# Kernel optimization log

Measured on AMD Instinct MI355X. Metric: run time of the kernel, lower is better.

## Reference

```python
import jax, jax.numpy as jnp
import numpy as np

IH, IW = 48, 48           # img_size
C = 256                   # inp == oup
NH, HD = 8, 32            # num_heads, head_dims; inner_dim = 256
HID = 4 * C               # MLP hidden
N = IH * IW               # window size (seq len) = 2304
SCALE = (C // NH) ** -0.5 # (inp_dims // num_heads) ** -0.5
EPS = 1e-5


def _relative_position_index():
    coords = np.stack(np.meshgrid(np.arange(IH), np.arange(IW), indexing='ij'))
    cf = coords.reshape(2, -1)
    rel = (cf[:, :, None] - cf[:, None, :]).transpose(1, 2, 0)
    rel[:, :, 0] += IH - 1
    rel[:, :, 1] += IW - 1
    rel[:, :, 0] *= 2 * IW - 1
    return jnp.asarray(rel.sum(-1).astype(np.int32))  # [N, N]


def setup_inputs() -> dict:
    key = jax.random.key(0)
    ks = jax.random.split(key, 12)
    s = 0.02
    return {
        'x': jax.random.normal(ks[0], (1, IH, IW, C), jnp.float32),
        'gamma1': jnp.ones((C,), jnp.float32),
        'beta1': jnp.zeros((C,), jnp.float32),
        'w_qkv': jax.random.normal(ks[1], (C, 3 * NH * HD), jnp.float32) * s,
        'w_proj': jax.random.normal(ks[2], (NH * HD, C), jnp.float32) * s,
        'b_proj': jnp.zeros((C,), jnp.float32),
        'bias_table': jax.random.normal(ks[3], ((2 * IH - 1) * (2 * IW - 1), NH), jnp.float32) * s,
        'gamma2': jnp.ones((C,), jnp.float32),
        'beta2': jnp.zeros((C,), jnp.float32),
        'w_fc1': jax.random.normal(ks[4], (C, HID), jnp.float32) * s,
        'b_fc1': jnp.zeros((HID,), jnp.float32),
        'w_fc2': jax.random.normal(ks[5], (HID, C), jnp.float32) * s,
        'b_fc2': jnp.zeros((C,), jnp.float32),
        'rel_idx': _relative_position_index(),
    }


def _layernorm(x, g, b):
    mu = jnp.mean(x, axis=-1, keepdims=True)
    var = jnp.mean(jnp.square(x - mu), axis=-1, keepdims=True)
    return (x - mu) * jax.lax.rsqrt(var + EPS) * g + b


def reference(x, gamma1, beta1, w_qkv, w_proj, b_proj, bias_table,
              gamma2, beta2, w_fc1, b_fc1, w_fc2, b_fc2, rel_idx):
    shortcut = x                                   # [1, IH, IW, C]
    t = x.reshape(1, N, C)
    t = _layernorm(t, gamma1, beta1)

    # qkv: [1, N, 3*NH*HD] -> q, k, v each [1, NH, N, HD]
    qkv = (t @ w_qkv).reshape(1, N, 3, NH, HD).transpose(2, 0, 3, 1, 4)
    q, k, v = qkv[0], qkv[1], qkv[2]
    q = q * SCALE

    attn = jnp.einsum('bhnd,bhmd->bhnm', q, k)     # [1, NH, N, N]
    # relative position bias: gather table rows by index -> [NH, N, N]
    bias = bias_table[rel_idx.reshape(-1)].reshape(N, N, NH).transpose(2, 0, 1)
    attn = jax.nn.softmax(attn + bias[None], axis=-1)

    o = jnp.einsum('bhnm,bhmd->bhnd', attn, v)     # [1, NH, N, HD]
    o = o.transpose(0, 2, 1, 3).reshape(1, N, NH * HD)
    o = o @ w_proj + b_proj                        # [1, N, C]

    x = shortcut + o.reshape(1, IH, IW, C)
    shortcut = x

    t = _layernorm(x.reshape(1, N, C), gamma2, beta2)
    t = jax.nn.gelu(t @ w_fc1 + b_fc1, approximate=False) @ w_fc2 + b_fc2
    return shortcut + t.reshape(1, IH, IW, C)
```

## Files before the change

kernel.cpp:

```cpp
#include <hip/hip_runtime.h>
#include <hip/hip_bf16.h>
#include <math.h>

#define IH 48
#define IW 48
#define NN 2304
#define CC 256
#define NH 8
#define HD 32
#define HID 1024
#define NBIAS 9025
#define SCALE 0.17677669529663687f
#define LOG2E 1.4426950408889634f
#define LN_EPS 1e-5f

typedef __attribute__((ext_vector_type(8))) short bf16x8;
typedef __attribute__((ext_vector_type(4))) float f32x4;

__device__ __forceinline__ short f2b(float f) {
    __hip_bfloat16 h = __float2bfloat16(f);
    short s; __builtin_memcpy(&s, &h, 2); return s;
}
__device__ __forceinline__ float b2f(short s) {
    __hip_bfloat16 h; __builtin_memcpy(&h, &s, 2); return __bfloat162float(h);
}
__device__ __forceinline__ float fast_exp2(float x) {
#if __has_builtin(__builtin_amdgcn_exp2f)
    return __builtin_amdgcn_exp2f(x);
#else
    return exp2f(x);
#endif
}

__global__ void prep_kernel(const float* __restrict__ x, const float* __restrict__ g,
                            const float* __restrict__ b, const float* __restrict__ bp,
                            short* __restrict__ t1, float* __restrict__ x2,
                            const float* __restrict__ w_qkv, const float* __restrict__ w_proj,
                            const float* __restrict__ w_fc1, const float* __restrict__ w_fc2,
                            const float* __restrict__ bt,
                            short* __restrict__ o_qkv, short* __restrict__ o_proj,
                            short* __restrict__ o_fc1, short* __restrict__ o_fc2,
                            short* __restrict__ o_bias)
{
    const int bid = blockIdx.x, tid = threadIdx.x;
    if (bid < NN) {
        __shared__ float red[8];
        float v = x[bid * CC + tid];
        float s = v, s2 = v * v;
        #pragma unroll
        for (int off = 32; off > 0; off >>= 1) {
            s  += __shfl_xor(s, off);
            s2 += __shfl_xor(s2, off);
        }
        const int wid = tid >> 6;
        if ((tid & 63) == 0) { red[wid * 2] = s; red[wid * 2 + 1] = s2; }
        __syncthreads();
        float tot  = red[0] + red[2] + red[4] + red[6];
        float tot2 = red[1] + red[3] + red[5] + red[7];
        float mu   = tot * (1.0f / CC);
        float var  = tot2 * (1.0f / CC) - mu * mu;
        float rstd = rsqrtf(var + LN_EPS);
        t1[bid * CC + tid] = f2b((v - mu) * rstd * g[tid] + b[tid]);
        x2[bid * CC + tid] = v + bp[tid];
        return;
    }
    const int stride = (gridDim.x - NN) * 256;
    for (int i = (bid - NN) * 256 + tid; i < 858632; i += stride) {
        int j = i;
        if (j < 196608)            { int n = j >> 8,  k = j & 255;  o_qkv [j] = f2b(w_qkv [k * 768  + n]); }
        else if ((j -= 196608) < 65536)  { int n = j >> 8,  k = j & 255;  o_proj[j] = f2b(w_proj[k * 256  + n]); }
        else if ((j -= 65536)  < 262144) { int n = j >> 8,  k = j & 255;  o_fc1 [j] = f2b(w_fc1 [k * 1024 + n]); }
        else if ((j -= 262144) < 262144) { int n = j >> 10, k = j & 1023; o_fc2 [j] = f2b(w_fc2 [k * 256  + n]); }
        else { j -= 262144; int h = j / NBIAS, idx = j - h * NBIAS; o_bias[j] = f2b(bt[idx * NH + h] * LOG2E); }
    }
}

__global__ void ln_kernel(const float* __restrict__ x,
                          const float* __restrict__ g,
                          const float* __restrict__ b,
                          const float* __restrict__ bfc2,
                          short* __restrict__ out_t,
                          float* __restrict__ out_base)
{
    __shared__ float red[8];
    const int row = blockIdx.x, tid = threadIdx.x;
    float v = x[row * CC + tid];
    float s = v, s2 = v * v;
    #pragma unroll
    for (int off = 32; off > 0; off >>= 1) {
        s  += __shfl_xor(s, off);
        s2 += __shfl_xor(s2, off);
    }
    const int wid = tid >> 6;
    if ((tid & 63) == 0) { red[wid * 2] = s; red[wid * 2 + 1] = s2; }
    __syncthreads();
    float tot  = red[0] + red[2] + red[4] + red[6];
    float tot2 = red[1] + red[3] + red[5] + red[7];
    float mu   = tot * (1.0f / CC);
    float var  = tot2 * (1.0f / CC) - mu * mu;
    float rstd = rsqrtf(var + LN_EPS);
    out_t[row * CC + tid] = f2b((v - mu) * rstd * g[tid] + b[tid]);
    out_base[row * CC + tid] = v + bfc2[tid];
}

#define GSTRIDE 72
template<int KLEN, int KSTR>
__device__ __forceinline__ void mfma_gemm_core(const short* __restrict__ A,
                                               const short* __restrict__ BT,
                                               int m0, int n0, int kb, f32x4 acc[4],
                                               short* lds)
{
    short* As = lds;
    short* Bs = lds + 64 * GSTRIDE;
    const int tid  = threadIdx.x;
    const int w    = tid >> 6, lane = tid & 63;
    const int quad = lane >> 4, l15 = lane & 15;
    const int sr = tid >> 2;
    const int sc = (tid & 3) * 16;
    #pragma unroll
    for (int c = 0; c < 4; ++c) acc[c] = (f32x4){0.f, 0.f, 0.f, 0.f};

    const short* Ap = &A [(m0 + sr) * KSTR + kb + sc];
    const short* Bp = &BT[(n0 + sr) * KSTR + kb + sc];
    bf16x8 ra0 = *(const bf16x8*)Ap,       ra1 = *(const bf16x8*)(Ap + 8);
    bf16x8 rb0 = *(const bf16x8*)Bp,       rb1 = *(const bf16x8*)(Bp + 8);

    for (int k0 = 0; k0 < KLEN; k0 += 64) {
        __syncthreads();
        *(bf16x8*)&As[sr * GSTRIDE + sc]     = ra0;
        *(bf16x8*)&As[sr * GSTRIDE + sc + 8] = ra1;
        *(bf16x8*)&Bs[sr * GSTRIDE + sc]     = rb0;
        *(bf16x8*)&Bs[sr * GSTRIDE + sc + 8] = rb1;
        if (k0 + 64 < KLEN) {
            ra0 = *(const bf16x8*)(Ap + k0 + 64);
            ra1 = *(const bf16x8*)(Ap + k0 + 72);
            rb0 = *(const bf16x8*)(Bp + k0 + 64);
            rb1 = *(const bf16x8*)(Bp + k0 + 72);
        }
        __syncthreads();
        #pragma unroll
        for (int s = 0; s < 2; ++s) {
            bf16x8 a = *(const bf16x8*)&As[(w * 16 + l15) * GSTRIDE + s * 32 + quad * 8];
            #pragma unroll
            for (int c = 0; c < 4; ++c) {
                bf16x8 b = *(const bf16x8*)&Bs[(c * 16 + l15) * GSTRIDE + s * 32 + quad * 8];
                acc[c] = __builtin_amdgcn_mfma_f32_16x16x32_bf16(a, b, acc[c], 0, 0, 0);
            }
        }
    }
}

__global__ void qkv_kernel(const short* __restrict__ t1, const short* __restrict__ wT,
                           short* __restrict__ qb, short* __restrict__ kb,
                           short* __restrict__ vT)
{
    __shared__ short lds[2 * 64 * GSTRIDE];
    f32x4 acc[4];
    const int m0 = blockIdx.y * 64, n0 = blockIdx.x * 64;
    mfma_gemm_core<256, 256>(t1, wT, m0, n0, 0, acc, lds);
    const int lane = threadIdx.x & 63, w = threadIdx.x >> 6;
    const int quad = lane >> 4, l15 = lane & 15;
    #pragma unroll
    for (int c = 0; c < 4; ++c) {
        int col = n0 + c * 16 + l15;
        int three = col >> 8, rem = col & 255;
        int h = rem >> 5, d = rem & 31;
        #pragma unroll
        for (int r = 0; r < 4; ++r) {
            int row = m0 + w * 16 + quad * 4 + r;
            float v = acc[c][r];
            if (three == 0)      qb[(h * NN + row) * HD + d] = f2b(v * (SCALE * LOG2E));
            else if (three == 1) kb[(h * NN + row) * HD + d] = f2b(v);
            else                 vT[(h * HD + d) * NN + row] = f2b(v);
        }
    }
}

#define PSTRIDE 40
__global__ __launch_bounds__(256) void attn_kernel(
        const short* __restrict__ qb, const short* __restrict__ kb,
        const short* __restrict__ vT, const short* __restrict__ biasT,
        short* __restrict__ o)
{
    __shared__ float Ored[4][16][33];
    __shared__ float lred[4][16];
    __shared__ short sbuf[4][16 * PSTRIDE];
    const int w = threadIdx.x >> 6, lane = threadIdx.x & 63;
    const int quad = lane >> 4, l15 = lane & 15;
    const int h = blockIdx.x / 144, q0 = (blockIdx.x % 144) * 16;
    const int t0 = w * 576;
    short* sb = &sbuf[w][0];
    const short* bt = &biasT[h * NBIAS];

    bf16x8 qf = *(const bf16x8*)&qb[(h * NN + q0 + l15) * HD + quad * 8];

    int base[4];
    #pragma unroll
    for (int r = 0; r < 4; ++r) {
        int row = q0 + quad * 4 + r;
        int qi = row / IW, qj = row % IW;
        base[r] = (qi + 47) * 95 + (qj + 47);
    }

    f32x4 O0 = (f32x4){0.f,0.f,0.f,0.f}, O1 = (f32x4){0.f,0.f,0.f,0.f};
    float lp[4] = {0.f, 0.f, 0.f, 0.f};
    const f32x4 zero = (f32x4){0.f,0.f,0.f,0.f};

    for (int c = 0; c < 18; ++c) {
        const int t = t0 + c * 32;
        bf16x8 k0f = *(const bf16x8*)&kb[(h * NN + t      + l15) * HD + quad * 8];
        bf16x8 k1f = *(const bf16x8*)&kb[(h * NN + t + 16 + l15) * HD + quad * 8];
        f32x4 s0 = __builtin_amdgcn_mfma_f32_16x16x32_bf16(qf, k0f, zero, 0, 0, 0);
        f32x4 s1 = __builtin_amdgcn_mfma_f32_16x16x32_bf16(qf, k1f, zero, 0, 0, 0);
        bf16x8 v0 = *(const bf16x8*)&vT[(h * HD + l15)      * NN + t + quad * 8];
        bf16x8 v1 = *(const bf16x8*)&vT[(h * HD + 16 + l15) * NN + t + quad * 8];

        int key0 = t + l15, key1 = t + 16 + l15;
        int boff0 = -((key0 / IW) * 95 + key0 % IW);
        int boff1 = -((key1 / IW) * 95 + key1 % IW);

        #pragma unroll
        for (int r = 0; r < 4; ++r) {
            float p0 = fast_exp2(s0[r] + b2f(bt[base[r] + boff0]));
            float p1 = fast_exp2(s1[r] + b2f(bt[base[r] + boff1]));
            lp[r] += p0 + p1;
            sb[(quad * 4 + r) * PSTRIDE + l15]      = f2b(p0);
            sb[(quad * 4 + r) * PSTRIDE + 16 + l15] = f2b(p1);
        }
        asm volatile("s_waitcnt lgkmcnt(0)" ::: "memory");
        bf16x8 pa = *(const bf16x8*)&sb[l15 * PSTRIDE + quad * 8];
        O0 = __builtin_amdgcn_mfma_f32_16x16x32_bf16(pa, v0, O0, 0, 0, 0);
        O1 = __builtin_amdgcn_mfma_f32_16x16x32_bf16(pa, v1, O1, 0, 0, 0);
    }

    #pragma unroll
    for (int r = 0; r < 4; ++r) {
        float l = lp[r];
        l += __shfl_xor(l, 1); l += __shfl_xor(l, 2);
        l += __shfl_xor(l, 4); l += __shfl_xor(l, 8);
        if (l15 == 0) lred[w][quad * 4 + r] = l;
        Ored[w][quad * 4 + r][l15]      = O0[r];
        Ored[w][quad * 4 + r][16 + l15] = O1[r];
    }
    __syncthreads();
    {
        const int col = threadIdx.x & 31;
        for (int rr = threadIdx.x >> 5; rr < 16; rr += 8) {
            float s = 0.f, l = 0.f;
            #pragma unroll
            for (int p = 0; p < 4; ++p) { s += Ored[p][rr][col]; l += lred[p][rr]; }
            o[(q0 + rr) * CC + h * HD + col] = f2b(s / l);
        }
    }
}

__global__ void proj_kernel(const short* __restrict__ o, const short* __restrict__ wT,
                            float* __restrict__ x2)
{
    __shared__ short lds[2 * 64 * GSTRIDE];
    f32x4 acc[4];
    const int m0 = blockIdx.y * 64, n0 = blockIdx.x * 64, kb = blockIdx.z * 128;
    mfma_gemm_core<128, 256>(o, wT, m0, n0, kb, acc, lds);
    const int lane = threadIdx.x & 63, w = threadIdx.x >> 6;
    const int quad = lane >> 4, l15 = lane & 15;
    #pragma unroll
    for (int c = 0; c < 4; ++c) {
        int col = n0 + c * 16 + l15;
        #pragma unroll
        for (int r = 0; r < 4; ++r) {
            int row = m0 + w * 16 + quad * 4 + r;
            atomicAdd(&x2[row * CC + col], acc[c][r]);
        }
    }
}

__global__ void fc1_kernel(const short* __restrict__ t2, const short* __restrict__ wT,
                           const float* __restrict__ bias, short* __restrict__ h1)
{
    __shared__ short lds[2 * 64 * GSTRIDE];
    f32x4 acc[4];
    const int m0 = blockIdx.y * 64, n0 = blockIdx.x * 64;
    mfma_gemm_core<256, 256>(t2, wT, m0, n0, 0, acc, lds);
    const int lane = threadIdx.x & 63, w = threadIdx.x >> 6;
    const int quad = lane >> 4, l15 = lane & 15;
    #pragma unroll
    for (int c = 0; c < 4; ++c) {
        int col = n0 + c * 16 + l15;
        #pragma unroll
        for (int r = 0; r < 4; ++r) {
            int row = m0 + w * 16 + quad * 4 + r;
            float v = acc[c][r] + bias[col];
            float ge = 0.5f * v * (1.0f + erff(v * 0.7071067811865476f));
            h1[row * HID + col] = f2b(ge);
        }
    }
}

__global__ void fc2_kernel(const short* __restrict__ h1, const short* __restrict__ wT,
                           float* __restrict__ out)
{
    __shared__ short lds[2 * 64 * GSTRIDE];
    f32x4 acc[4];
    const int m0 = blockIdx.y * 64, n0 = blockIdx.x * 64, kb = blockIdx.z * 512;
    mfma_gemm_core<512, 1024>(h1, wT, m0, n0, kb, acc, lds);
    const int lane = threadIdx.x & 63, w = threadIdx.x >> 6;
    const int quad = lane >> 4, l15 = lane & 15;
    #pragma unroll
    for (int c = 0; c < 4; ++c) {
        int col = n0 + c * 16 + l15;
        #pragma unroll
        for (int r = 0; r < 4; ++r) {
            int row = m0 + w * 16 + quad * 4 + r;
            atomicAdd(&out[row * CC + col], acc[c][r]);
        }
    }
}

extern "C" void kernel_launch(void* const* d_in, const int* in_sizes, int n_in,
                              void* d_out, int out_size, void* d_ws, size_t ws_size,
                              hipStream_t stream)
{
    const float* x          = (const float*)d_in[0];
    const float* gamma1     = (const float*)d_in[1];
    const float* beta1      = (const float*)d_in[2];
    const float* w_qkv      = (const float*)d_in[3];
    const float* w_proj     = (const float*)d_in[4];
    const float* b_proj     = (const float*)d_in[5];
    const float* bias_table = (const float*)d_in[6];
    const float* gamma2     = (const float*)d_in[7];
    const float* beta2      = (const float*)d_in[8];
    const float* w_fc1      = (const float*)d_in[9];
    const float* b_fc1      = (const float*)d_in[10];
    const float* w_fc2      = (const float*)d_in[11];
    const float* b_fc2      = (const float*)d_in[12];

    short* S = (short*)d_ws;
    const int NC = NN * CC;
    short* t1     = S;
    short* qb     = t1  + NC;
    short* kb     = qb  + NC;
    short* vT     = kb  + NC;
    short* obuf   = vT  + NC;
    short* t2     = obuf+ NC;
    short* h1     = t2  + NC;
    short* wTqkv  = h1  + NN * HID;
    short* wTproj = wTqkv  + 768 * 256;
    short* wTfc1  = wTproj + 256 * 256;
    short* wTfc2  = wTfc1  + 1024 * 256;
    short* biasT  = wTfc2  + 256 * 1024;
    float* x2     = (float*)(biasT + NH * NBIAS + 8);

    prep_kernel<<<NN + 512, 256, 0, stream>>>(x, gamma1, beta1, b_proj, t1, x2,
                                              w_qkv, w_proj, w_fc1, w_fc2, bias_table,
                                              wTqkv, wTproj, wTfc1, wTfc2, biasT);
    qkv_kernel<<<dim3(12, 36), 256, 0, stream>>>(t1, wTqkv, qb, kb, vT);
    attn_kernel<<<1152, 256, 0, stream>>>(qb, kb, vT, biasT, obuf);
    proj_kernel<<<dim3(4, 36, 2), 256, 0, stream>>>(obuf, wTproj, x2);
    ln_kernel<<<NN, 256, 0, stream>>>(x2, gamma2, beta2, b_fc2, t2, (float*)d_out);
    fc1_kernel<<<dim3(16, 36), 256, 0, stream>>>(t2, wTfc1, b_fc1, h1);
    fc2_kernel<<<dim3(4, 36, 2), 256, 0, stream>>>(h1, wTfc2, (float*)d_out);
}
```

Baseline: 170.9 us.

## Tile weight transposes, cache bias window in LDS, replace split-K atomics with partials

Weight transposition moves into its own kernel that goes through a shared-memory tile, so both reads and writes are coalesced instead of strided. The bias-table transpose now reads the table contiguously. The attention kernel stages the per-query-row window of relative-position bias in LDS, replacing scattered global gathers and per-key div/mod work with LDS lookups. The split-K proj and fc2 GEMMs now write separate partial buffers instead of issuing float atomics, and the partials are summed in the LN kernel and a new reduction kernel. The cost is one extra launch and extra partial-buffer traffic, and the partial buffers alias the t1/qb/kb/vT workspace region.

Result: no change. 169.1 us (-1.1%).

```diff
diff --git a/kernel.cpp b/kernel.cpp
--- a/kernel.cpp
+++ b/kernel.cpp
@@ -33,14 +33,8 @@
 }
 
 __global__ void prep_kernel(const float* __restrict__ x, const float* __restrict__ g,
-                            const float* __restrict__ b, const float* __restrict__ bp,
-                            short* __restrict__ t1, float* __restrict__ x2,
-                            const float* __restrict__ w_qkv, const float* __restrict__ w_proj,
-                            const float* __restrict__ w_fc1, const float* __restrict__ w_fc2,
-                            const float* __restrict__ bt,
-                            short* __restrict__ o_qkv, short* __restrict__ o_proj,
-                            short* __restrict__ o_fc1, short* __restrict__ o_fc2,
-                            short* __restrict__ o_bias)
+                            const float* __restrict__ b, short* __restrict__ t1,
+                            const float* __restrict__ bt, short* __restrict__ o_bias)
 {
     const int bid = blockIdx.x, tid = threadIdx.x;
     if (bid < NN) {
@@ -61,30 +55,48 @@
         float var  = tot2 * (1.0f / CC) - mu * mu;
         float rstd = rsqrtf(var + LN_EPS);
         t1[bid * CC + tid] = f2b((v - mu) * rstd * g[tid] + b[tid]);
-        x2[bid * CC + tid] = v + bp[tid];
         return;
     }
     const int stride = (gridDim.x - NN) * 256;
-    for (int i = (bid - NN) * 256 + tid; i < 858632; i += stride) {
-        int j = i;
-        if (j < 196608)            { int n = j >> 8,  k = j & 255;  o_qkv [j] = f2b(w_qkv [k * 768  + n]); }
-        else if ((j -= 196608) < 65536)  { int n = j >> 8,  k = j & 255;  o_proj[j] = f2b(w_proj[k * 256  + n]); }
-        else if ((j -= 65536)  < 262144) { int n = j >> 8,  k = j & 255;  o_fc1 [j] = f2b(w_fc1 [k * 1024 + n]); }
-        else if ((j -= 262144) < 262144) { int n = j >> 10, k = j & 1023; o_fc2 [j] = f2b(w_fc2 [k * 256  + n]); }
-        else { j -= 262144; int h = j / NBIAS, idx = j - h * NBIAS; o_bias[j] = f2b(bt[idx * NH + h] * LOG2E); }
-    }
-}
-
-__global__ void ln_kernel(const float* __restrict__ x,
-                          const float* __restrict__ g,
-                          const float* __restrict__ b,
-                          const float* __restrict__ bfc2,
-                          short* __restrict__ out_t,
-                          float* __restrict__ out_base)
+    for (int i = (bid - NN) * 256 + tid; i < NBIAS * NH; i += stride) {
+        int idx = i >> 3, h = i & 7;
+        o_bias[h * NBIAS + idx] = f2b(bt[i] * LOG2E);
+    }
+}
+
+__global__ void wtrans_kernel(const float* __restrict__ w_qkv, const float* __restrict__ w_proj,
+                              const float* __restrict__ w_fc1, const float* __restrict__ w_fc2,
+                              short* __restrict__ o_qkv, short* __restrict__ o_proj,
+                              short* __restrict__ o_fc1, short* __restrict__ o_fc2)
+{
+    __shared__ float t[32][33];
+    int b = blockIdx.x;
+    const float* src; short* dst; int K, Nn, kt, nt;
+    if (b < 192)      { src = w_qkv;  dst = o_qkv;  K = 256;  Nn = 768;  kt = b / 24; nt = b % 24; }
+    else if (b < 256) { b -= 192; src = w_proj; dst = o_proj; K = 256;  Nn = 256;  kt = b / 8;  nt = b % 8; }
+    else if (b < 512) { b -= 256; src = w_fc1;  dst = o_fc1;  K = 256;  Nn = 1024; kt = b / 32; nt = b % 32; }
+    else              { b -= 512; src = w_fc2;  dst = o_fc2;  K = 1024; Nn = 256;  kt = b / 8;  nt = b % 8; }
+    const int r = threadIdx.x >> 5, c = threadIdx.x & 31;
+    const int k0 = kt * 32, n0 = nt * 32;
+    #pragma unroll
+    for (int i = 0; i < 4; ++i)
+        t[r + i * 8][c] = src[(k0 + r + i * 8) * Nn + n0 + c];
+    __syncthreads();
+    #pragma unroll
+    for (int i = 0; i < 4; ++i)
+        dst[(n0 + r + i * 8) * K + k0 + c] = f2b(t[c][r + i * 8]);
+}
+
+__global__ void ln_kernel(const float* __restrict__ p0, const float* __restrict__ p1,
+                          const float* __restrict__ bp, const float* __restrict__ x_in,
+                          const float* __restrict__ g, const float* __restrict__ b,
+                          short* __restrict__ t2, float* __restrict__ x2)
 {
     __shared__ float red[8];
     const int row = blockIdx.x, tid = threadIdx.x;
-    float v = x[row * CC + tid];
+    const int i = row * CC + tid;
+    float v = p0[i] + p1[i] + bp[tid] + x_in[i];
+    x2[i] = v;
     float s = v, s2 = v * v;
     #pragma unroll
     for (int off = 32; off > 0; off >>= 1) {
@@ -99,8 +111,7 @@
     float mu   = tot * (1.0f / CC);
     float var  = tot2 * (1.0f / CC) - mu * mu;
     float rstd = rsqrtf(var + LN_EPS);
-    out_t[row * CC + tid] = f2b((v - mu) * rstd * g[tid] + b[tid]);
-    out_base[row * CC + tid] = v + bfc2[tid];
+    t2[i] = f2b((v - mu) * rstd * g[tid] + b[tid]);
 }
 
 #define GSTRIDE 72
@@ -185,6 +196,7 @@
     __shared__ float Ored[4][16][33];
     __shared__ float lred[4][16];
     __shared__ short sbuf[4][16 * PSTRIDE];
+    __shared__ short bwin[48][64];
     const int w = threadIdx.x >> 6, lane = threadIdx.x & 63;
     const int quad = lane >> 4, l15 = lane & 15;
     const int h = blockIdx.x / 144, q0 = (blockIdx.x % 144) * 16;
@@ -192,19 +204,20 @@
     short* sb = &sbuf[w][0];
     const short* bt = &biasT[h * NBIAS];
 
+    const int qi = q0 / IW, qj0 = q0 % IW;
+
+    for (int idx = threadIdx.x; idx < 48 * 63; idx += 256) {
+        int kr = idx / 63, cc = idx - kr * 63;
+        bwin[kr][cc] = bt[(qi - kr + 47) * 95 + qj0 + cc];
+    }
+
     bf16x8 qf = *(const bf16x8*)&qb[(h * NN + q0 + l15) * HD + quad * 8];
-
-    int base[4];
-    #pragma unroll
-    for (int r = 0; r < 4; ++r) {
-        int row = q0 + quad * 4 + r;
-        int qi = row / IW, qj = row % IW;
-        base[r] = (qi + 47) * 95 + (qj + 47);
-    }
 
     f32x4 O0 = (f32x4){0.f,0.f,0.f,0.f}, O1 = (f32x4){0.f,0.f,0.f,0.f};
     float lp[4] = {0.f, 0.f, 0.f, 0.f};
     const f32x4 zero = (f32x4){0.f,0.f,0.f,0.f};
+
+    __syncthreads();
 
     for (int c = 0; c < 18; ++c) {
         const int t = t0 + c * 32;
@@ -215,14 +228,15 @@
         bf16x8 v0 = *(const bf16x8*)&vT[(h * HD + l15)      * NN + t + quad * 8];
         bf16x8 v1 = *(const bf16x8*)&vT[(h * HD + 16 + l15) * NN + t + quad * 8];
 
-        int key0 = t + l15, key1 = t + 16 + l15;
-        int boff0 = -((key0 / IW) * 95 + key0 % IW);
-        int boff1 = -((key1 / IW) * 95 + key1 % IW);
-
-        #pragma unroll
-        for (int r = 0; r < 4; ++r) {
-            float p0 = fast_exp2(s0[r] + b2f(bt[base[r] + boff0]));
-            float p1 = fast_exp2(s1[r] + b2f(bt[base[r] + boff1]));
+        const int ki0 = t / IW,        kj0_ = t - ki0 * IW;
+        const int ki1 = (t + 16) / IW, kj1_ = (t + 16) - ki1 * IW;
+        const int cA = quad * 4 + 47 - kj0_ - l15;
+        const int cB = quad * 4 + 47 - kj1_ - l15;
+
+        #pragma unroll
+        for (int r = 0; r < 4; ++r) {
+            float p0 = fast_exp2(s0[r] + b2f(bwin[ki0][cA + r]));
+            float p1 = fast_exp2(s1[r] + b2f(bwin[ki1][cB + r]));
             lp[r] += p0 + p1;
             sb[(quad * 4 + r) * PSTRIDE + l15]      = f2b(p0);
             sb[(quad * 4 + r) * PSTRIDE + 16 + l15] = f2b(p1);
@@ -248,28 +262,29 @@
         for (int rr = threadIdx.x >> 5; rr < 16; rr += 8) {
             float s = 0.f, l = 0.f;
             #pragma unroll
-            for (int p = 0; p < 4; ++p) { s += Ored[p][rr][col]; l += lred[p][rr]; }
+            for (int pw = 0; pw < 4; ++pw) { s += Ored[pw][rr][col]; l += lred[pw][rr]; }
             o[(q0 + rr) * CC + h * HD + col] = f2b(s / l);
         }
     }
 }
 
 __global__ void proj_kernel(const short* __restrict__ o, const short* __restrict__ wT,
-                            float* __restrict__ x2)
+                            float* __restrict__ Ppj)
 {
     __shared__ short lds[2 * 64 * GSTRIDE];
     f32x4 acc[4];
-    const int m0 = blockIdx.y * 64, n0 = blockIdx.x * 64, kb = blockIdx.z * 128;
-    mfma_gemm_core<128, 256>(o, wT, m0, n0, kb, acc, lds);
+    const int m0 = blockIdx.y * 64, n0 = blockIdx.x * 64, z = blockIdx.z;
+    mfma_gemm_core<128, 256>(o, wT, m0, n0, z * 128, acc, lds);
     const int lane = threadIdx.x & 63, w = threadIdx.x >> 6;
     const int quad = lane >> 4, l15 = lane & 15;
+    float* out = Ppj + z * (NN * CC);
     #pragma unroll
     for (int c = 0; c < 4; ++c) {
         int col = n0 + c * 16 + l15;
         #pragma unroll
         for (int r = 0; r < 4; ++r) {
             int row = m0 + w * 16 + quad * 4 + r;
-            atomicAdd(&x2[row * CC + col], acc[c][r]);
+            out[row * CC + col] = acc[c][r];
         }
     }
 }
@@ -297,23 +312,32 @@
 }
 
 __global__ void fc2_kernel(const short* __restrict__ h1, const short* __restrict__ wT,
-                           float* __restrict__ out)
+                           float* __restrict__ Pfc)
 {
     __shared__ short lds[2 * 64 * GSTRIDE];
     f32x4 acc[4];
-    const int m0 = blockIdx.y * 64, n0 = blockIdx.x * 64, kb = blockIdx.z * 512;
-    mfma_gemm_core<512, 1024>(h1, wT, m0, n0, kb, acc, lds);
+    const int m0 = blockIdx.y * 64, n0 = blockIdx.x * 64, z = blockIdx.z;
+    mfma_gemm_core<512, 1024>(h1, wT, m0, n0, z * 512, acc, lds);
     const int lane = threadIdx.x & 63, w = threadIdx.x >> 6;
     const int quad = lane >> 4, l15 = lane & 15;
+    float* out = Pfc + z * (NN * CC);
     #pragma unroll
     for (int c = 0; c < 4; ++c) {
         int col = n0 + c * 16 + l15;
         #pragma unroll
         for (int r = 0; r < 4; ++r) {
             int row = m0 + w * 16 + quad * 4 + r;
-            atomicAdd(&out[row * CC + col], acc[c][r]);
-        }
-    }
+            out[row * CC + col] = acc[c][r];
+        }
+    }
+}
+
+__global__ void fc2_red(const float* __restrict__ Pfc, const float* __restrict__ bias,
+                        const float* __restrict__ x2, float* __restrict__ out)
+{
+    const int i = blockIdx.x * CC + threadIdx.x;
+    const int NC = NN * CC;
+    out[i] = Pfc[i] + Pfc[NC + i] + bias[threadIdx.x] + x2[i];
 }
 
 extern "C" void kernel_launch(void* const* d_in, const int* in_sizes, int n_in,
@@ -349,14 +373,19 @@
     short* wTfc2  = wTfc1  + 1024 * 256;
     short* biasT  = wTfc2  + 256 * 1024;
     float* x2     = (float*)(biasT + NH * NBIAS + 8);
-
-    prep_kernel<<<NN + 512, 256, 0, stream>>>(x, gamma1, beta1, b_proj, t1, x2,
-                                              w_qkv, w_proj, w_fc1, w_fc2, bias_table,
-                                              wTqkv, wTproj, wTfc1, wTfc2, biasT);
+    float* Ppj    = (float*)t1;
+    float* Pfc    = (float*)t1;
+
+    prep_kernel<<<NN + 64, 256, 0, stream>>>(x, gamma1, beta1, t1,
+                                             bias_table, biasT);
+    wtrans_kernel<<<768, 256, 0, stream>>>(w_qkv, w_proj, w_fc1, w_fc2,
+                                           wTqkv, wTproj, wTfc1, wTfc2);
     qkv_kernel<<<dim3(12, 36), 256, 0, stream>>>(t1, wTqkv, qb, kb, vT);
     attn_kernel<<<1152, 256, 0, stream>>>(qb, kb, vT, biasT, obuf);
-    proj_kernel<<<dim3(4, 36, 2), 256, 0, stream>>>(obuf, wTproj, x2);
-    ln_kernel<<<NN, 256, 0, stream>>>(x2, gamma2, beta2, b_fc2, t2, (float*)d_out);
+    proj_kernel<<<dim3(4, 36, 2), 256, 0, stream>>>(obuf, wTproj, Ppj);
+    ln_kernel<<<NN, 256, 0, stream>>>(Ppj, Ppj + NC, b_proj, x,
+                                      gamma2, beta2, t2, x2);
     fc1_kernel<<<dim3(16, 36), 256, 0, stream>>>(t2, wTfc1, b_fc1, h1);
-    fc2_kernel<<<dim3(4, 36, 2), 256, 0, stream>>>(h1, wTfc2, (float*)d_out);
-}
+    fc2_kernel<<<dim3(4, 36, 2), 256, 0, stream>>>(h1, wTfc2, Pfc);
+    fc2_red<<<NN, 256, 0, stream>>>(Pfc, b_fc2, x2, (float*)d_out);
+}
```
